# Performance work log

Measured on AMD Instinct MI355X. Metric: run time of the kernel, lower is better.

## Reference

```python
import jax, jax.numpy as jnp
import numpy as np
from jax.scipy.special import erf, erfinv

N = 1024
B = 262144
SQRT6 = float(np.sqrt(6.0))
SQRT3 = float(np.sqrt(3.0))


def setup_inputs() -> dict:
    key = jax.random.key(0)
    x = jax.random.normal(key, (B, 1), dtype=jnp.float32)
    centers = (jnp.arange(N, dtype=jnp.float32) / N + 1.0 / (2 * N))  # [N]
    return {"x": x, "centers": centers}


def _cdf_y(v):
    # CDF_Y(y) = 0.5*erf(sqrt(3)*erfinv(2y-1)) + 0.5
    return 0.5 * erf(SQRT3 * erfinv(2.0 * v - 1.0)) + 0.5


def reference(x, centers):
    n = centers.shape[0]
    # companding transform: y in (0,1), shape [B,1]
    y = 0.5 * erf(x / SQRT6) + 0.5
    # brute-force nearest-uniform-center search: [B,N]
    mse = (y - centers[None, :]) ** 2
    indices = jnp.argmin(mse, axis=1)            # [B] int
    y_hat = centers[indices][:, None]            # [B,1]
    x_hat = SQRT6 * erfinv(2.0 * y_hat - 1.0)    # [B,1]
    k = indices.astype(jnp.float32)
    likelihood = _cdf_y((k + 1.0) / n) - _cdf_y(k / n)  # [B]
    return (x_hat, likelihood, y_hat)
```

## Files before the change

kernel.cpp:

```cpp
#include <hip/hip_runtime.h>
#include <math.h>


#define B_ELEMS 262144
#define NC      1024

#define INV_SQRT6 0.40824829046386302f
#define SQRT6     2.4494897427831781f
#define SQRT3     1.7320508075688772f

__global__ __launch_bounds__(1024) void build_tables_kernel(
        float* __restrict__ xh_tab, float* __restrict__ lik_tab) {
    __shared__ float cdf[NC + 1];
    const int k = threadIdx.x;

    float c;
    if (k == 0) {
        c = 0.0f;
    } else {
        float v = (float)k * (1.0f / (float)NC);
        c = fmaf(0.5f, erff(SQRT3 * erfinvf(fmaf(v, 2.0f, -1.0f))), 0.5f);
    }
    cdf[k] = c;
    if (k == NC - 1) cdf[NC] = 1.0f;

    float yh = ((float)k + 0.5f) * (1.0f / (float)NC);
    xh_tab[k] = SQRT6 * erfinvf(fmaf(yh, 2.0f, -1.0f));

    __syncthreads();
    lik_tab[k] = cdf[k + 1] - cdf[k];
}

__global__ __launch_bounds__(256) void compand_kernel(
        const float* __restrict__ x, float* __restrict__ out,
        const float* __restrict__ xh_tab, const float* __restrict__ lik_tab) {
    __shared__ float s_xh[NC];
    __shared__ float s_lik[NC];
    const int t = threadIdx.x;

    ((float4*)s_xh)[t]  = ((const float4*)xh_tab)[t];
    ((float4*)s_lik)[t] = ((const float4*)lik_tab)[t];
    __syncthreads();

    const int i = blockIdx.x * 256 + t;
    float xv = x[i];
    float y  = fmaf(0.5f, erff(xv * INV_SQRT6), 0.5f);
    int k = (int)floorf(y * (float)NC);
    k = max(0, min(NC - 1, k));

    out[i]               = s_xh[k];
    out[B_ELEMS + i]     = s_lik[k];
    out[2 * B_ELEMS + i] = ((float)k + 0.5f) * (1.0f / (float)NC);
}

extern "C" void kernel_launch(void* const* d_in, const int* in_sizes, int n_in,
                              void* d_out, int out_size, void* d_ws, size_t ws_size,
                              hipStream_t stream) {
    const float* x = (const float*)d_in[0];
    float* out = (float*)d_out;

    float* xh_tab  = (float*)d_ws;
    float* lik_tab = (float*)d_ws + NC;

    build_tables_kernel<<<1, NC, 0, stream>>>(xh_tab, lik_tab);

    dim3 block(256);
    dim3 grid(B_ELEMS / 256);
    compand_kernel<<<grid, block, 0, stream>>>(x, out, xh_tab, lik_tab);
}
```

Before: 58.12 us.

## Fuse table construction into compand kernel and process two elements per thread

Drops the separate single-block table-building kernel. Each block now recomputes the CDF and x_hat tables in shared memory (4 entries per thread) before doing the lookups. Each thread handles two inputs with float2 loads and stores, which halves the number of blocks, and floorf is replaced by a plain truncating cast. This removes a kernel launch and the serial dependency on a one-block kernel, at the cost of redundant erfinv/erf work in every block.

Result: no change. 58.32 us (+0.3%).

```diff
diff --git a/kernel.cpp b/kernel.cpp
--- a/kernel.cpp
+++ b/kernel.cpp
@@ -4,53 +4,54 @@
 
 #define B_ELEMS 262144
 #define NC      1024
+#define THREADS 256
+#define EPT     2
+#define BLOCKS  (B_ELEMS / (THREADS * EPT))
 
 #define INV_SQRT6 0.40824829046386302f
 #define SQRT6     2.4494897427831781f
 #define SQRT3     1.7320508075688772f
 
-__global__ __launch_bounds__(1024) void build_tables_kernel(
-        float* __restrict__ xh_tab, float* __restrict__ lik_tab) {
-    __shared__ float cdf[NC + 1];
-    const int k = threadIdx.x;
-
-    float c;
-    if (k == 0) {
-        c = 0.0f;
-    } else {
-        float v = (float)k * (1.0f / (float)NC);
-        c = fmaf(0.5f, erff(SQRT3 * erfinvf(fmaf(v, 2.0f, -1.0f))), 0.5f);
-    }
-    cdf[k] = c;
-    if (k == NC - 1) cdf[NC] = 1.0f;
-
-    float yh = ((float)k + 0.5f) * (1.0f / (float)NC);
-    xh_tab[k] = SQRT6 * erfinvf(fmaf(yh, 2.0f, -1.0f));
-
-    __syncthreads();
-    lik_tab[k] = cdf[k + 1] - cdf[k];
-}
-
-__global__ __launch_bounds__(256) void compand_kernel(
-        const float* __restrict__ x, float* __restrict__ out,
-        const float* __restrict__ xh_tab, const float* __restrict__ lik_tab) {
+__global__ __launch_bounds__(THREADS) void compand_fused_kernel(
+        const float* __restrict__ x, float* __restrict__ out) {
+    __shared__ float s_cdf[NC + 1];
     __shared__ float s_xh[NC];
-    __shared__ float s_lik[NC];
     const int t = threadIdx.x;
 
-    ((float4*)s_xh)[t]  = ((const float4*)xh_tab)[t];
-    ((float4*)s_lik)[t] = ((const float4*)lik_tab)[t];
+    const int i = (blockIdx.x * THREADS + t) * EPT;
+    const float2 xv = *(const float2*)(x + i);
+
+#pragma unroll
+    for (int r = 0; r < 4; ++r) {
+        const int k = t * 4 + r;
+        float c;
+        if (k == 0) {
+            c = 0.0f;
+        } else {
+            const float v = (float)k * (1.0f / (float)NC);
+            c = fmaf(0.5f, erff(SQRT3 * erfinvf(fmaf(v, 2.0f, -1.0f))), 0.5f);
+        }
+        s_cdf[k] = c;
+
+        const float yh = ((float)k + 0.5f) * (1.0f / (float)NC);
+        s_xh[k] = SQRT6 * erfinvf(fmaf(yh, 2.0f, -1.0f));
+    }
+    if (t == 0) s_cdf[NC] = 1.0f;
     __syncthreads();
 
-    const int i = blockIdx.x * 256 + t;
-    float xv = x[i];
-    float y  = fmaf(0.5f, erff(xv * INV_SQRT6), 0.5f);
-    int k = (int)floorf(y * (float)NC);
-    k = max(0, min(NC - 1, k));
+    const float y0 = fmaf(0.5f, erff(xv.x * INV_SQRT6), 0.5f);
+    const float y1 = fmaf(0.5f, erff(xv.y * INV_SQRT6), 0.5f);
+    int k0 = (int)(y0 * (float)NC);
+    int k1 = (int)(y1 * (float)NC);
+    k0 = max(0, min(NC - 1, k0));
+    k1 = max(0, min(NC - 1, k1));
 
-    out[i]               = s_xh[k];
-    out[B_ELEMS + i]     = s_lik[k];
-    out[2 * B_ELEMS + i] = ((float)k + 0.5f) * (1.0f / (float)NC);
+    *(float2*)(out + i) = make_float2(s_xh[k0], s_xh[k1]);
+    *(float2*)(out + B_ELEMS + i) =
+        make_float2(s_cdf[k0 + 1] - s_cdf[k0], s_cdf[k1 + 1] - s_cdf[k1]);
+    *(float2*)(out + 2 * B_ELEMS + i) =
+        make_float2(((float)k0 + 0.5f) * (1.0f / (float)NC),
+                    ((float)k1 + 0.5f) * (1.0f / (float)NC));
 }
 
 extern "C" void kernel_launch(void* const* d_in, const int* in_sizes, int n_in,
@@ -58,13 +59,7 @@
                               hipStream_t stream) {
     const float* x = (const float*)d_in[0];
     float* out = (float*)d_out;
+    (void)d_ws; (void)ws_size;
 
-    float* xh_tab  = (float*)d_ws;
-    float* lik_tab = (float*)d_ws + NC;
-
-    build_tables_kernel<<<1, NC, 0, stream>>>(xh_tab, lik_tab);
-
-    dim3 block(256);
-    dim3 grid(B_ELEMS / 256);
-    compand_kernel<<<grid, block, 0, stream>>>(x, out, xh_tab, lik_tab);
+    compand_fused_kernel<<<dim3(BLOCKS), dim3(THREADS), 0, stream>>>(x, out);
 }
```
